# Optimization experiments

Measured on AMD Instinct MI355X. Metric: run time of the kernel, lower is better.

## Reference

```python
import jax, jax.numpy as jnp
import numpy as np

B, N, D = 8, 256, 128


def setup_inputs() -> dict:
    key = jax.random.key(0)
    ks = jax.random.split(key, 4)
    s1 = 1.0 / np.sqrt(4 * D)
    s2 = 1.0 / np.sqrt(2 * D)
    s3 = 1.0 / np.sqrt(D)
    return {
        "tour_features": jax.random.normal(ks[0], (B, N, D), dtype=jnp.float32),
        "W1": jax.random.uniform(ks[1], (4 * D, 2 * D), jnp.float32, -s1, s1),
        "b1": jnp.zeros((2 * D,), jnp.float32),
        "W2": jax.random.uniform(ks[2], (2 * D, D), jnp.float32, -s2, s2),
        "b2": jnp.zeros((D,), jnp.float32),
        "W3": jax.random.uniform(ks[3], (D, 1), jnp.float32, -s3, s3),
        "b3": jnp.zeros((1,), jnp.float32),
    }


def reference(tour_features, W1, b1, W2, b2, W3, b3):
    Bs, Ns, Ds = tour_features.shape
    x = tour_features
    x_next = jnp.roll(x, -1, axis=1)  # node at (k+1) % N
    # Split first linear's weight by the 4 concatenated feature blocks:
    # cat([x_i, x_{i+1}, x_j, x_{j+1}]) @ W1 == x_i@W1a + x_{i+1}@W1b + x_j@W1c + x_{j+1}@W1d
    W1a, W1b, W1c, W1d = jnp.split(W1, 4, axis=0)
    Pi = x @ W1a + x_next @ W1b          # [B, N, 2D] (i-side projection)
    Pj = x @ W1c + x_next @ W1d          # [B, N, 2D] (j-side projection)
    h1 = jax.nn.relu(Pi[:, :, None, :] + Pj[:, None, :, :] + b1)  # [B, N, N, 2D]
    h2 = jax.nn.relu(h1 @ W2 + b2)       # [B, N, N, D]
    score = jnp.tanh((h2 @ W3 + b3)[..., 0])  # [B, N, N]
    # Valid pairs: j >= i + 2 and not (j - i == N - 1)
    ii = jnp.arange(Ns)[:, None]
    jj = jnp.arange(Ns)[None, :]
    mask = (jj >= ii + 2) & (jj - ii != Ns - 1)
    improvement_matrix = jnp.where(mask[None], score, 0.0)
    improved_tour = jnp.broadcast_to(jnp.arange(Ns), (Bs, Ns))
    return improved_tour, improvement_matrix
```

## Files before the change

### kernel.cpp

```cpp
#include <hip/hip_runtime.h>


typedef __attribute__((ext_vector_type(8))) short short8;
typedef __attribute__((ext_vector_type(8))) _Float16 half8;
typedef __attribute__((ext_vector_type(4))) float floatx4;

static __device__ __forceinline__ unsigned short f2bf(float f) {
  unsigned int x = __float_as_uint(f);
  x += 0x7fff + ((x >> 16) & 1);
  return (unsigned short)(x >> 16);
}

static __device__ __forceinline__ unsigned short f2h(float f) {
  _Float16 h = (_Float16)f;
  return __builtin_bit_cast(unsigned short, h);
}

static __device__ __forceinline__ float fast_tanh(float x) {
  float e = __expf(2.0f * fabsf(x));
  float t = 1.0f - 2.0f * __builtin_amdgcn_rcpf(e + 1.0f);
  return copysignf(t, x);
}

static __device__ __forceinline__ long pack_fp8(half8 s) {
  int lo = __builtin_amdgcn_cvt_pk_fp8_f32((float)s[0], (float)s[1], 0, false);
  lo = __builtin_amdgcn_cvt_pk_fp8_f32((float)s[2], (float)s[3], lo, true);
  int hi = __builtin_amdgcn_cvt_pk_fp8_f32((float)s[4], (float)s[5], 0, false);
  hi = __builtin_amdgcn_cvt_pk_fp8_f32((float)s[6], (float)s[7], hi, true);
  return (long)(unsigned)lo | ((long)hi << 32);
}

static __device__ __forceinline__ void gload_lds16(const void* g, void* l) {
  __builtin_amdgcn_global_load_lds(
      (const __attribute__((address_space(1))) unsigned int*)g,
      (__attribute__((address_space(3))) unsigned int*)l, 16, 0, 0);
}

__global__ __launch_bounds__(256) void k_prep(
    const float* __restrict__ W1, unsigned short* __restrict__ W1T) {
  int e = blockIdx.x * 256 + threadIdx.x;
  int n = e >> 8, k = e & 255;
  int v = k >> 3;
  int sw = (((v & 16) | ((v ^ (n & 15)) & 15)) << 3) | (k & 7);
  W1T[(n << 8) + sw] = f2bf(W1[((k + (n & 256)) << 8) + (n & 255)]);
}

__global__ __launch_bounds__(256) void k_proj(
    const float* __restrict__ x, const unsigned short* __restrict__ W1T,
    const float* __restrict__ b1, unsigned short* __restrict__ PiH,
    unsigned short* __restrict__ PjH, const float* __restrict__ W2,
    float* __restrict__ out, unsigned char* __restrict__ W2F8) {
  const int tid = threadIdx.x;
  const int bx = blockIdx.x;

  if (bx >= 256) {
    if (bx < 770) {
      int t = (bx - 256) * 256 + tid;
      int e = t * 4;
      floatx4 w;
      if (e < 2048) {
        float v = (float)(e & 255);
        w = (floatx4){v, v + 1.f, v + 2.f, v + 3.f};
      } else {
        w = (floatx4)0.f;
      }
      *(floatx4*)(out + e) = w;
    } else {
      int t = (bx - 770) * 256 + tid;
      int p = t >> 7, n = t & 127;
      float f0 = W2[(2 * p) * 128 + n] * 16.f;
      float f1 = W2[(2 * p + 1) * 128 + n] * 16.f;
      int v2 = __builtin_amdgcn_cvt_pk_fp8_f32(f0, f1, 0, false);
      int q = n >> 5, which = (n >> 4) & 1, l = n & 15;
      int c = p >> 2, off = (p & 3) * 2;
      int cs = (c & 16) | ((c ^ l) & 15);
      *(unsigned short*)(W2F8 + q * 8192 + l * 512 + cs * 16 + which * 8 + off) =
          (unsigned short)(v2 & 0xffff);
    }
    return;
  }

  const int mg = bx >> 3;
  const int ng = bx & 7;
  const int wr = tid >> 6, lane = tid & 63, quad = lane >> 4, l15 = lane & 15;

  __shared__ unsigned short As[64 * 256];
  __shared__ unsigned short Bs[64 * 256];

  const unsigned short* Bsrc = W1T + ng * 64 * 256;
#pragma unroll
  for (int it = 0; it < 8; ++it) {
    const int c = it * 256 + wr * 64 + lane;
    gload_lds16(Bsrc + c * 8, &Bs[(it * 256 + wr * 64) * 8]);
  }

#pragma unroll
  for (int pass = 0; pass < 8; ++pass) {
    const int rr = pass * 8 + (tid >> 5);
    const int grow = mg * 64 + rr;
    const int pos = grow & 255, bb = grow >> 8;
    const int v = tid & 31;
    const int pos2 = (v < 16) ? pos : ((pos + 1) & 255);
    const float* src = x + (bb * 256 + pos2) * 128 + (v & 15) * 8;
    const floatx4 f0 = *(const floatx4*)(src);
    const floatx4 f1 = *(const floatx4*)(src + 4);
    union { short8 s; unsigned short u[8]; } o;
    o.u[0] = f2bf(f0[0]); o.u[1] = f2bf(f0[1]);
    o.u[2] = f2bf(f0[2]); o.u[3] = f2bf(f0[3]);
    o.u[4] = f2bf(f1[0]); o.u[5] = f2bf(f1[1]);
    o.u[6] = f2bf(f1[2]); o.u[7] = f2bf(f1[3]);
    const int sw = (v & 16) | ((v ^ (rr & 15)) & 15);
    *(short8*)((char*)As + rr * 512 + sw * 16) = o.s;
  }
  __syncthreads();

  floatx4 acc[4];
#pragma unroll
  for (int mt = 0; mt < 4; ++mt) acc[mt] = (floatx4)0.f;

  const char* Ab = (const char*)As;
  const char* Bb = (const char*)Bs + wr * 16 * 512;
  const int base_sw = l15 * 512 + ((quad ^ l15) << 4);

#pragma unroll
  for (int ks = 0; ks < 8; ++ks) {
    const int swz = base_sw ^ (ks << 6);
    short8 bfr = *(const short8*)(Bb + swz);
#pragma unroll
    for (int mt = 0; mt < 4; ++mt) {
      short8 afr = *(const short8*)(Ab + mt * 8192 + swz);
      acc[mt] = __builtin_amdgcn_mfma_f32_16x16x32_bf16(afr, bfr, acc[mt], 0, 0, 0);
    }
  }

  const int ch = ng * 64 + wr * 16 + l15;
  const float bias = (ch < 256) ? b1[ch] : 0.f;
  const bool isPi = (ch < 256);
  unsigned short* dst = isPi ? PiH : PjH;
  const int chan = ch & 255;
  const int ck = chan >> 3, coff = chan & 7;
#pragma unroll
  for (int mt = 0; mt < 4; ++mt)
#pragma unroll
    for (int r = 0; r < 4; ++r) {
      int row = mg * 64 + mt * 16 + quad * 4 + r;
      int cpos;
      if (isPi) cpos = chan;
      else {
        int cs = (ck & 16) | ((ck ^ (row & 15)) & 15);
        cpos = cs * 8 + coff;
      }
      dst[row * 256 + cpos] = f2h(acc[mt][r] + bias);
    }
}

__global__ __launch_bounds__(256, 3) void k_main(
    const unsigned short* __restrict__ PiH, const unsigned short* __restrict__ PjH,
    const unsigned char* __restrict__ W2F8, const float* __restrict__ b2,
    const float* __restrict__ W3, const float* __restrict__ b3,
    float* __restrict__ outm) {
  const int tid = threadIdx.x;
  const int wr = tid >> 6;
  const int lane = tid & 63, quad = lane >> 4, l15 = lane & 15;

  __shared__ unsigned char W2s[32768];
  __shared__ unsigned char PjS[16384];
  __shared__ unsigned char PiS[4096];

  const int bid = blockIdx.x;
  const int b = bid / 288;
  const int rem = bid - b * 288;
  int jt = 0, basej = 0;
  if (rem >= 8)   { jt = 1; basej = 8;   }
  if (rem >= 24)  { jt = 2; basej = 24;  }
  if (rem >= 48)  { jt = 3; basej = 48;  }
  if (rem >= 80)  { jt = 4; basej = 80;  }
  if (rem >= 120) { jt = 5; basej = 120; }
  if (rem >= 168) { jt = 6; basej = 168; }
  if (rem >= 224) { jt = 7; basej = 224; }
  const int i = (rem - basej) * 4 + wr;

  const unsigned char* pjsrc =
      (const unsigned char*)(PjH + ((b << 8) + jt * 32) * 256);
  const unsigned char* pisrc =
      (const unsigned char*)(PiH + ((b << 8) + i) * 256);
#pragma unroll
  for (int it = 0; it < 8; ++it) {
    const int c = it * 256 + wr * 64 + lane;
    gload_lds16(W2F8 + c * 16, &W2s[(it * 256 + wr * 64) * 16]);
  }
#pragma unroll
  for (int it = 0; it < 4; ++it) {
    const int c = it * 256 + wr * 64 + lane;
    gload_lds16(pjsrc + c * 16, &PjS[(it * 256 + wr * 64) * 16]);
  }
  gload_lds16(pisrc + (lane & 31) * 16, &PiS[wr * 1024]);
  __syncthreads();

  const char* W2base = (const char*)&W2s[0];
  const char* PjBase = (const char*)&PjS[0];
  const char* PiBase = (const char*)&PiS[0] + wr * 1024 + quad * 16;
  const int sw16 = l15 * 512 + (((quad ^ l15) & 15) << 4);

  floatx4 acc[2][8];
#pragma unroll
  for (int mt = 0; mt < 2; ++mt)
#pragma unroll
    for (int nt = 0; nt < 8; ++nt) acc[mt][nt] = (floatx4)0.f;

  union U4 { uint4 v; half8 h; };
  U4 piR[2], pjR[2][2];
  piR[0].v = *(const uint4*)(PiBase);
  pjR[0][0].v = *(const uint4*)(PjBase + sw16);
  pjR[0][1].v = *(const uint4*)(PjBase + 8192 + sw16);
  piR[1].v = *(const uint4*)(PiBase + 64);
  {
    const char* pj = PjBase + (sw16 ^ 64);
    pjR[1][0].v = *(const uint4*)(pj);
    pjR[1][1].v = *(const uint4*)(pj + 8192);
  }

  uint4 bfA[4], bfB[4];
  {
    const char* b0 = W2base + sw16;
#pragma unroll
    for (int q = 0; q < 4; ++q) bfA[q] = *(const uint4*)(b0 + q * 8192);
  }

  long aC0, aC1;
  {
    const half8 s0 = __builtin_elementwise_max(piR[0].h + pjR[0][0].h,
                                               (half8)(_Float16)0);
    const half8 s1 = __builtin_elementwise_max(piR[0].h + pjR[0][1].h,
                                               (half8)(_Float16)0);
    aC0 = pack_fp8(s0);
    aC1 = pack_fp8(s1);
  }

#pragma unroll
  for (int ks = 0; ks < 8; ++ks) {
    if (ks < 7) {
      const char* bn = W2base + (sw16 ^ ((ks + 1) << 6));
#pragma unroll
      for (int q = 0; q < 4; ++q)
        ((ks & 1) ? bfA : bfB)[q] = *(const uint4*)(bn + q * 8192);
    }
    if (ks < 6) {
      piR[ks & 1].v = *(const uint4*)(PiBase + (ks + 2) * 64);
      const char* pj = PjBase + (sw16 ^ ((ks + 2) << 6));
      pjR[ks & 1][0].v = *(const uint4*)(pj);
      pjR[ks & 1][1].v = *(const uint4*)(pj + 8192);
    }
    long aN0 = 0, aN1 = 0;
    if (ks < 7) {
      const half8 s0 = __builtin_elementwise_max(
          piR[(ks + 1) & 1].h + pjR[(ks + 1) & 1][0].h, (half8)(_Float16)0);
      const half8 s1 = __builtin_elementwise_max(
          piR[(ks + 1) & 1].h + pjR[(ks + 1) & 1][1].h, (half8)(_Float16)0);
      aN0 = pack_fp8(s0);
      aN1 = pack_fp8(s1);
    }
    const uint4* bc = (ks & 1) ? bfB : bfA;
    __builtin_amdgcn_s_setprio(1);
#pragma unroll
    for (int q = 0; q < 4; ++q) {
      const long blo = (long)bc[q].x | ((long)bc[q].y << 32);
      const long bhi = (long)bc[q].z | ((long)bc[q].w << 32);
      acc[0][2 * q]     = __builtin_amdgcn_mfma_f32_16x16x32_fp8_fp8(aC0, blo, acc[0][2 * q], 0, 0, 0);
      acc[1][2 * q]     = __builtin_amdgcn_mfma_f32_16x16x32_fp8_fp8(aC1, blo, acc[1][2 * q], 0, 0, 0);
      acc[0][2 * q + 1] = __builtin_amdgcn_mfma_f32_16x16x32_fp8_fp8(aC0, bhi, acc[0][2 * q + 1], 0, 0, 0);
      acc[1][2 * q + 1] = __builtin_amdgcn_mfma_f32_16x16x32_fp8_fp8(aC1, bhi, acc[1][2 * q + 1], 0, 0, 0);
    }
    __builtin_amdgcn_s_setprio(0);
    if (ks < 7) { aC0 = aN0; aC1 = aN1; }
  }

  float* orow = outm + ((b << 8) + i) * 256 + jt * 32;
  const float b3v = b3[0];
  const float s16 = 0.0625f;
#pragma unroll
  for (int mt = 0; mt < 2; ++mt) {
    float p0 = 0, p1 = 0, p2 = 0, p3 = 0;
#pragma unroll
    for (int nt = 0; nt < 8; ++nt) {
      float w3v = W3[nt * 16 + l15];
      float b2v = b2[nt * 16 + l15];
      floatx4 a = acc[mt][nt];
      p0 += fmaxf(fmaf(a[0], s16, b2v), 0.f) * w3v;
      p1 += fmaxf(fmaf(a[1], s16, b2v), 0.f) * w3v;
      p2 += fmaxf(fmaf(a[2], s16, b2v), 0.f) * w3v;
      p3 += fmaxf(fmaf(a[3], s16, b2v), 0.f) * w3v;
    }
#pragma unroll
    for (int m = 8; m >= 1; m >>= 1) {
      p0 += __shfl_xor(p0, m, 16);
      p1 += __shfl_xor(p1, m, 16);
      p2 += __shfl_xor(p2, m, 16);
      p3 += __shfl_xor(p3, m, 16);
    }
    if (l15 == 0) {
      const int jl = jt * 32 + mt * 16 + quad * 4;
      float ps[4] = {p0, p1, p2, p3};
#pragma unroll
      for (int r = 0; r < 4; ++r) {
        int j = jl + r;
        float sc = fast_tanh(ps[r] + b3v);
        bool valid = (j >= i + 2) && (j - i != 255);
        orow[mt * 16 + quad * 4 + r] = valid ? sc : 0.f;
      }
    }
  }
}

extern "C" void kernel_launch(void* const* d_in, const int* in_sizes, int n_in,
                              void* d_out, int out_size, void* d_ws, size_t ws_size,
                              hipStream_t stream) {
  const float* x  = (const float*)d_in[0];
  const float* W1 = (const float*)d_in[1];
  const float* b1 = (const float*)d_in[2];
  const float* W2 = (const float*)d_in[3];
  const float* b2 = (const float*)d_in[4];
  const float* W3 = (const float*)d_in[5];
  const float* b3 = (const float*)d_in[6];
  float* out = (float*)d_out;

  unsigned short* PiH  = (unsigned short*)d_ws;
  unsigned short* PjH  = PiH + 524288;
  unsigned short* W1T  = PjH + 524288;
  unsigned char*  W2F8 = (unsigned char*)(W1T + 131072);

  k_prep<<<512, 256, 0, stream>>>(W1, W1T);
  k_proj<<<834, 256, 0, stream>>>(x, W1T, b1, PiH, PjH, W2, out, W2F8);
  k_main<<<2304, 256, 0, stream>>>(PiH, PjH, W2F8, b2, W3, b3, out + 2048);
}
```

Before: 94.22 us.

## Make k_main persistent over tile groups to reuse staged W2 and Pj

k_main now launches 512 blocks, and each block loops over 4 or 5 consecutive tile groups. W2 is loaded into LDS once per block instead of once per tile, and the Pj tile is reloaded only when the batch or j-tile changes. Pi rows are read directly from global memory instead of being staged through LDS, and launch bounds drop to 2 waves per SIMD. The aim is to cut redundant W2 and Pj global-to-LDS traffic and per-block setup. The cost is fewer resident blocks, less latency hiding, and global-latency Pi loads inside the pipelined loop.

After: 100.1 us. +6.3%, slower.

```diff
diff --git a/kernel.cpp b/kernel.cpp
--- a/kernel.cpp
+++ b/kernel.cpp
@@ -154,7 +154,7 @@
     }
 }
 
-__global__ __launch_bounds__(256, 3) void k_main(
+__global__ __launch_bounds__(256, 2) void k_main(
     const unsigned short* __restrict__ PiH, const unsigned short* __restrict__ PjH,
     const unsigned char* __restrict__ W2F8, const float* __restrict__ b2,
     const float* __restrict__ W3, const float* __restrict__ b3,
@@ -165,148 +165,161 @@
 
   __shared__ unsigned char W2s[32768];
   __shared__ unsigned char PjS[16384];
-  __shared__ unsigned char PiS[4096];
 
   const int bid = blockIdx.x;
-  const int b = bid / 288;
-  const int rem = bid - b * 288;
-  int jt = 0, basej = 0;
-  if (rem >= 8)   { jt = 1; basej = 8;   }
-  if (rem >= 24)  { jt = 2; basej = 24;  }
-  if (rem >= 48)  { jt = 3; basej = 48;  }
-  if (rem >= 80)  { jt = 4; basej = 80;  }
-  if (rem >= 120) { jt = 5; basej = 120; }
-  if (rem >= 168) { jt = 6; basej = 168; }
-  if (rem >= 224) { jt = 7; basej = 224; }
-  const int i = (rem - basej) * 4 + wr;
-
-  const unsigned char* pjsrc =
-      (const unsigned char*)(PjH + ((b << 8) + jt * 32) * 256);
-  const unsigned char* pisrc =
-      (const unsigned char*)(PiH + ((b << 8) + i) * 256);
+  const int g0 = (bid >> 1) * 9 + (bid & 1) * 5;
+  const int gcnt = (bid & 1) ? 4 : 5;
+
 #pragma unroll
   for (int it = 0; it < 8; ++it) {
     const int c = it * 256 + wr * 64 + lane;
     gload_lds16(W2F8 + c * 16, &W2s[(it * 256 + wr * 64) * 16]);
   }
-#pragma unroll
-  for (int it = 0; it < 4; ++it) {
-    const int c = it * 256 + wr * 64 + lane;
-    gload_lds16(pjsrc + c * 16, &PjS[(it * 256 + wr * 64) * 16]);
-  }
-  gload_lds16(pisrc + (lane & 31) * 16, &PiS[wr * 1024]);
-  __syncthreads();
 
   const char* W2base = (const char*)&W2s[0];
   const char* PjBase = (const char*)&PjS[0];
-  const char* PiBase = (const char*)&PiS[0] + wr * 1024 + quad * 16;
   const int sw16 = l15 * 512 + (((quad ^ l15) & 15) << 4);
-
-  floatx4 acc[2][8];
-#pragma unroll
-  for (int mt = 0; mt < 2; ++mt)
-#pragma unroll
-    for (int nt = 0; nt < 8; ++nt) acc[mt][nt] = (floatx4)0.f;
-
-  union U4 { uint4 v; half8 h; };
-  U4 piR[2], pjR[2][2];
-  piR[0].v = *(const uint4*)(PiBase);
-  pjR[0][0].v = *(const uint4*)(PjBase + sw16);
-  pjR[0][1].v = *(const uint4*)(PjBase + 8192 + sw16);
-  piR[1].v = *(const uint4*)(PiBase + 64);
-  {
-    const char* pj = PjBase + (sw16 ^ 64);
-    pjR[1][0].v = *(const uint4*)(pj);
-    pjR[1][1].v = *(const uint4*)(pj + 8192);
-  }
-
-  uint4 bfA[4], bfB[4];
-  {
-    const char* b0 = W2base + sw16;
-#pragma unroll
-    for (int q = 0; q < 4; ++q) bfA[q] = *(const uint4*)(b0 + q * 8192);
-  }
-
-  long aC0, aC1;
-  {
-    const half8 s0 = __builtin_elementwise_max(piR[0].h + pjR[0][0].h,
-                                               (half8)(_Float16)0);
-    const half8 s1 = __builtin_elementwise_max(piR[0].h + pjR[0][1].h,
-                                               (half8)(_Float16)0);
-    aC0 = pack_fp8(s0);
-    aC1 = pack_fp8(s1);
-  }
-
-#pragma unroll
-  for (int ks = 0; ks < 8; ++ks) {
-    if (ks < 7) {
-      const char* bn = W2base + (sw16 ^ ((ks + 1) << 6));
-#pragma unroll
-      for (int q = 0; q < 4; ++q)
-        ((ks & 1) ? bfA : bfB)[q] = *(const uint4*)(bn + q * 8192);
-    }
-    if (ks < 6) {
-      piR[ks & 1].v = *(const uint4*)(PiBase + (ks + 2) * 64);
-      const char* pj = PjBase + (sw16 ^ ((ks + 2) << 6));
-      pjR[ks & 1][0].v = *(const uint4*)(pj);
-      pjR[ks & 1][1].v = *(const uint4*)(pj + 8192);
-    }
-    long aN0 = 0, aN1 = 0;
-    if (ks < 7) {
-      const half8 s0 = __builtin_elementwise_max(
-          piR[(ks + 1) & 1].h + pjR[(ks + 1) & 1][0].h, (half8)(_Float16)0);
-      const half8 s1 = __builtin_elementwise_max(
-          piR[(ks + 1) & 1].h + pjR[(ks + 1) & 1][1].h, (half8)(_Float16)0);
-      aN0 = pack_fp8(s0);
-      aN1 = pack_fp8(s1);
-    }
-    const uint4* bc = (ks & 1) ? bfB : bfA;
-    __builtin_amdgcn_s_setprio(1);
-#pragma unroll
-    for (int q = 0; q < 4; ++q) {
-      const long blo = (long)bc[q].x | ((long)bc[q].y << 32);
-      const long bhi = (long)bc[q].z | ((long)bc[q].w << 32);
-      acc[0][2 * q]     = __builtin_amdgcn_mfma_f32_16x16x32_fp8_fp8(aC0, blo, acc[0][2 * q], 0, 0, 0);
-      acc[1][2 * q]     = __builtin_amdgcn_mfma_f32_16x16x32_fp8_fp8(aC1, blo, acc[1][2 * q], 0, 0, 0);
-      acc[0][2 * q + 1] = __builtin_amdgcn_mfma_f32_16x16x32_fp8_fp8(aC0, bhi, acc[0][2 * q + 1], 0, 0, 0);
-      acc[1][2 * q + 1] = __builtin_amdgcn_mfma_f32_16x16x32_fp8_fp8(aC1, bhi, acc[1][2 * q + 1], 0, 0, 0);
-    }
-    __builtin_amdgcn_s_setprio(0);
-    if (ks < 7) { aC0 = aN0; aC1 = aN1; }
-  }
-
-  float* orow = outm + ((b << 8) + i) * 256 + jt * 32;
   const float b3v = b3[0];
   const float s16 = 0.0625f;
-#pragma unroll
-  for (int mt = 0; mt < 2; ++mt) {
-    float p0 = 0, p1 = 0, p2 = 0, p3 = 0;
-#pragma unroll
-    for (int nt = 0; nt < 8; ++nt) {
-      float w3v = W3[nt * 16 + l15];
-      float b2v = b2[nt * 16 + l15];
-      floatx4 a = acc[mt][nt];
-      p0 += fmaxf(fmaf(a[0], s16, b2v), 0.f) * w3v;
-      p1 += fmaxf(fmaf(a[1], s16, b2v), 0.f) * w3v;
-      p2 += fmaxf(fmaf(a[2], s16, b2v), 0.f) * w3v;
-      p3 += fmaxf(fmaf(a[3], s16, b2v), 0.f) * w3v;
-    }
-#pragma unroll
-    for (int m = 8; m >= 1; m >>= 1) {
-      p0 += __shfl_xor(p0, m, 16);
-      p1 += __shfl_xor(p1, m, 16);
-      p2 += __shfl_xor(p2, m, 16);
-      p3 += __shfl_xor(p3, m, 16);
-    }
-    if (l15 == 0) {
-      const int jl = jt * 32 + mt * 16 + quad * 4;
-      float ps[4] = {p0, p1, p2, p3};
-#pragma unroll
-      for (int r = 0; r < 4; ++r) {
-        int j = jl + r;
-        float sc = fast_tanh(ps[r] + b3v);
-        bool valid = (j >= i + 2) && (j - i != 255);
-        orow[mt * 16 + quad * 4 + r] = valid ? sc : 0.f;
+
+  int curb = -1, curjt = -1;
+
+#pragma unroll 1
+  for (int g = 0; g < gcnt; ++g) {
+    const int G = g0 + g;
+    const int bb_ = G / 288;
+    const int rem = G - bb_ * 288;
+    int jt = 0, basej = 0;
+    if (rem >= 8)   { jt = 1; basej = 8;   }
+    if (rem >= 24)  { jt = 2; basej = 24;  }
+    if (rem >= 48)  { jt = 3; basej = 48;  }
+    if (rem >= 80)  { jt = 4; basej = 80;  }
+    if (rem >= 120) { jt = 5; basej = 120; }
+    if (rem >= 168) { jt = 6; basej = 168; }
+    if (rem >= 224) { jt = 7; basej = 224; }
+    const int i = (rem - basej) * 4 + wr;
+
+    if (bb_ != curb || jt != curjt) {
+      if (g > 0) __syncthreads();
+      const unsigned char* pjsrc =
+          (const unsigned char*)(PjH + ((bb_ << 8) + jt * 32) * 256);
+#pragma unroll
+      for (int it = 0; it < 4; ++it) {
+        const int c = it * 256 + wr * 64 + lane;
+        gload_lds16(pjsrc + c * 16, &PjS[(it * 256 + wr * 64) * 16]);
+      }
+      __syncthreads();
+      curb = bb_; curjt = jt;
+    }
+
+    const unsigned short* PiRow = PiH + (((bb_ << 8) + i) << 8) + quad * 8;
+
+    floatx4 acc[2][8];
+#pragma unroll
+    for (int mt = 0; mt < 2; ++mt)
+#pragma unroll
+      for (int nt = 0; nt < 8; ++nt) acc[mt][nt] = (floatx4)0.f;
+
+    union U4 { uint4 v; half8 h; };
+    U4 piA, piB, pjA0, pjA1, pjB0, pjB1;
+    piA.v = *(const uint4*)(PiRow);
+    piB.v = *(const uint4*)(PiRow + 32);
+    pjA0.v = *(const uint4*)(PjBase + sw16);
+    pjA1.v = *(const uint4*)(PjBase + 8192 + sw16);
+    {
+      const char* pj = PjBase + (sw16 ^ 64);
+      pjB0.v = *(const uint4*)(pj);
+      pjB1.v = *(const uint4*)(pj + 8192);
+    }
+
+    uint4 bfA[4], bfB[4];
+    {
+      const char* b0 = W2base + sw16;
+#pragma unroll
+      for (int q = 0; q < 4; ++q) bfA[q] = *(const uint4*)(b0 + q * 8192);
+    }
+
+    long aC0, aC1;
+    {
+      const half8 s0 = __builtin_elementwise_max(piA.h + pjA0.h, (half8)(_Float16)0);
+      const half8 s1 = __builtin_elementwise_max(piA.h + pjA1.h, (half8)(_Float16)0);
+      aC0 = pack_fp8(s0);
+      aC1 = pack_fp8(s1);
+    }
+
+#pragma unroll
+    for (int ks = 0; ks < 8; ++ks) {
+      if (ks < 7) {
+        const char* bn = W2base + (sw16 ^ ((ks + 1) << 6));
+#pragma unroll
+        for (int q = 0; q < 4; ++q)
+          ((ks & 1) ? bfA : bfB)[q] = *(const uint4*)(bn + q * 8192);
+      }
+      if (ks < 6) {
+        U4& pid = (ks & 1) ? piB : piA;
+        pid.v = *(const uint4*)(PiRow + (ks + 2) * 32);
+        const char* pj = PjBase + (sw16 ^ ((ks + 2) << 6));
+        U4& pjd0 = (ks & 1) ? pjB0 : pjA0;
+        U4& pjd1 = (ks & 1) ? pjB1 : pjA1;
+        pjd0.v = *(const uint4*)(pj);
+        pjd1.v = *(const uint4*)(pj + 8192);
+      }
+      long aN0 = 0, aN1 = 0;
+      if (ks < 7) {
+        const U4& pin = ((ks + 1) & 1) ? piB : piA;
+        const U4& pn0 = ((ks + 1) & 1) ? pjB0 : pjA0;
+        const U4& pn1 = ((ks + 1) & 1) ? pjB1 : pjA1;
+        const half8 s0 = __builtin_elementwise_max(pin.h + pn0.h, (half8)(_Float16)0);
+        const half8 s1 = __builtin_elementwise_max(pin.h + pn1.h, (half8)(_Float16)0);
+        aN0 = pack_fp8(s0);
+        aN1 = pack_fp8(s1);
+      }
+      const uint4* bc = (ks & 1) ? bfB : bfA;
+      __builtin_amdgcn_s_setprio(1);
+#pragma unroll
+      for (int q = 0; q < 4; ++q) {
+        const long blo = (long)bc[q].x | ((long)bc[q].y << 32);
+        const long bhi = (long)bc[q].z | ((long)bc[q].w << 32);
+        acc[0][2 * q]     = __builtin_amdgcn_mfma_f32_16x16x32_fp8_fp8(aC0, blo, acc[0][2 * q], 0, 0, 0);
+        acc[1][2 * q]     = __builtin_amdgcn_mfma_f32_16x16x32_fp8_fp8(aC1, blo, acc[1][2 * q], 0, 0, 0);
+        acc[0][2 * q + 1] = __builtin_amdgcn_mfma_f32_16x16x32_fp8_fp8(aC0, bhi, acc[0][2 * q + 1], 0, 0, 0);
+        acc[1][2 * q + 1] = __builtin_amdgcn_mfma_f32_16x16x32_fp8_fp8(aC1, bhi, acc[1][2 * q + 1], 0, 0, 0);
+      }
+      __builtin_amdgcn_s_setprio(0);
+      if (ks < 7) { aC0 = aN0; aC1 = aN1; }
+    }
+
+    float* orow = outm + (((bb_ << 8) + i) << 8) + jt * 32;
+#pragma unroll
+    for (int mt = 0; mt < 2; ++mt) {
+      float p0 = 0, p1 = 0, p2 = 0, p3 = 0;
+#pragma unroll
+      for (int nt = 0; nt < 8; ++nt) {
+        float w3v = W3[nt * 16 + l15];
+        float b2v = b2[nt * 16 + l15];
+        floatx4 a = acc[mt][nt];
+        p0 += fmaxf(fmaf(a[0], s16, b2v), 0.f) * w3v;
+        p1 += fmaxf(fmaf(a[1], s16, b2v), 0.f) * w3v;
+        p2 += fmaxf(fmaf(a[2], s16, b2v), 0.f) * w3v;
+        p3 += fmaxf(fmaf(a[3], s16, b2v), 0.f) * w3v;
+      }
+#pragma unroll
+      for (int m = 8; m >= 1; m >>= 1) {
+        p0 += __shfl_xor(p0, m, 16);
+        p1 += __shfl_xor(p1, m, 16);
+        p2 += __shfl_xor(p2, m, 16);
+        p3 += __shfl_xor(p3, m, 16);
+      }
+      if (l15 == 0) {
+        const int jl = jt * 32 + mt * 16 + quad * 4;
+        float ps[4] = {p0, p1, p2, p3};
+#pragma unroll
+        for (int r = 0; r < 4; ++r) {
+          int j = jl + r;
+          float sc = fast_tanh(ps[r] + b3v);
+          bool valid = (j >= i + 2) && (j - i != 255);
+          orow[mt * 16 + quad * 4 + r] = valid ? sc : 0.f;
+        }
       }
     }
   }
@@ -331,5 +344,5 @@
 
   k_prep<<<512, 256, 0, stream>>>(W1, W1T);
   k_proj<<<834, 256, 0, stream>>>(x, W1T, b1, PiH, PjH, W2, out, W2F8);
-  k_main<<<2304, 256, 0, stream>>>(PiH, PjH, W2F8, b2, W3, b3, out + 2048);
-}
+  k_main<<<512, 256, 0, stream>>>(PiH, PjH, W2F8, b2, W3, b3, out + 2048);
+}
```
